# Kernel optimization log

Measured on AMD Instinct MI355X. Metric: run time of the kernel, lower is better.

## Reference

```python
import jax, jax.numpy as jnp
import numpy as np

# Model config (matches init_kwargs)
B, I, H, C = 2048, 1024, 2048, 1000   # batch, input_dim, hidden_dim, num_classes
S = 8                                  # num_wavefunctions
TOPK = 256
PARTIAL_NORM = 1.0
SM_STEPS = 2                           # self_modulation_steps
EPS = 1e-8


def setup_inputs() -> dict:
    key = jax.random.key(0)
    ks = jax.random.split(key, 9)
    x      = jax.random.normal(ks[0], (B, I), jnp.float32)
    # stacked per-wavefunction Linear(input_dim, 2*hidden_dim)
    W      = jax.random.normal(ks[1], (S, 2 * H, I), jnp.float32) * (1.0 / np.sqrt(I))
    b      = jax.random.normal(ks[2], (S, 2 * H), jnp.float32) * 0.01
    phases = jax.random.normal(ks[3], (S, H), jnp.float32) * 0.1   # phase_per_dim=True
    gate_W = jax.random.normal(ks[4], (H, H), jnp.float32) * (1.0 / np.sqrt(H))
    gate_b = jax.random.normal(ks[5], (H,), jnp.float32) * 0.01
    clf_W  = jax.random.normal(ks[6], (C, H), jnp.float32) * (1.0 / np.sqrt(H))
    clf_b  = jax.random.normal(ks[7], (C,), jnp.float32) * 0.01
    return {"x": x, "W": W, "b": b, "phases": phases,
            "gate_W": gate_W, "gate_b": gate_b, "clf_W": clf_W, "clf_b": clf_b}


def reference(x, W, b, phases, gate_W, gate_b, clf_W, clf_b):
    # All wavefunction branches batched into one GEMM: [B,S,2H]
    out = jnp.einsum('bi,shi->bsh', x, W) + b[None]
    out = jnp.exp(-(out * out))                      # ArcBell activation
    alpha, beta = out[..., :H], out[..., H:]         # [B,S,H] each
    norm_sq = jnp.sum(alpha * alpha + beta * beta, axis=-1, keepdims=True) + EPS
    factor = jnp.sqrt((PARTIAL_NORM * PARTIAL_NORM) / norm_sq)  # [B,S,1]
    alpha = alpha * factor
    beta = beta * factor
    cphi = jnp.cos(phases)[None]                     # [1,S,H]
    sphi = jnp.sin(phases)[None]
    # phase rotation + complex accumulate over wavefunctions
    sup_real = jnp.sum(alpha * cphi - beta * sphi, axis=1)   # [B,H]
    sup_imag = jnp.sum(alpha * sphi + beta * cphi, axis=1)
    # self-modulation (fixed small step count -> Python loop is fine)
    for _ in range(SM_STEPS):
        mag = jnp.sqrt(sup_real * sup_real + sup_imag * sup_imag)
        gate = jax.nn.sigmoid(mag @ gate_W.T + gate_b)
        sup_real = sup_real * gate
        sup_imag = sup_imag * gate
    mag_sq = sup_real * sup_real + sup_imag * sup_imag       # [B,H]
    # top-k masked probability aggregation
    _, idx = jax.lax.top_k(mag_sq, TOPK)                     # idx: [B,TOPK]
    mask = jnp.zeros_like(mag_sq).at[jnp.arange(B)[:, None], idx].set(1.0)
    masked = mag_sq * mask
    probs = masked / (jnp.sum(masked, axis=-1, keepdims=True) + EPS)
    logits = probs @ clf_W.T + clf_b                         # [B,C]
    return logits
```

## Files before the change

### kernel.cpp

```cpp
#include <hip/hip_runtime.h>

typedef _Float16 f16;
typedef _Float16 f16x8 __attribute__((ext_vector_type(8)));
typedef _Float16 f16x4 __attribute__((ext_vector_type(4)));
typedef float f32x4 __attribute__((ext_vector_type(4)));

#define B_    2048
#define I_    1024
#define H_    2048
#define C_    1000
#define S_    8
#define N1    32768
#define TOPK_ 256

__device__ __forceinline__ void gload16(const void* g, void* l) {
  __builtin_amdgcn_global_load_lds((const __attribute__((address_space(1))) void*)g,
                                   (__attribute__((address_space(3))) void*)l,
                                   16, 0, 0);
}

__global__ void cvt8_kernel(const float* __restrict__ src, f16* __restrict__ dst, int n8) {
  int i = blockIdx.x * blockDim.x + threadIdx.x;
  if (i >= n8) return;
  const float4 a = reinterpret_cast<const float4*>(src)[2 * i];
  const float4 b = reinterpret_cast<const float4*>(src)[2 * i + 1];
  f16x8 o = { (f16)a.x, (f16)a.y, (f16)a.z, (f16)a.w,
              (f16)b.x, (f16)b.y, (f16)b.z, (f16)b.w };
  reinterpret_cast<f16x8*>(dst)[i] = o;
}

__global__ void cvt_clf_kernel(const float* __restrict__ src, f16* __restrict__ dst) {
  int i = blockIdx.x * blockDim.x + threadIdx.x;
  if (i >= (1024 * H_ / 8)) return;
  f16x8 o;
  if (i < (C_ * H_ / 8)) {
    const float4 a = reinterpret_cast<const float4*>(src)[2 * i];
    const float4 b = reinterpret_cast<const float4*>(src)[2 * i + 1];
    o = (f16x8){ (f16)a.x, (f16)a.y, (f16)a.z, (f16)a.w,
                 (f16)b.x, (f16)b.y, (f16)b.z, (f16)b.w };
  } else {
    o = (f16x8){ (f16)0.f, (f16)0.f, (f16)0.f, (f16)0.f,
                 (f16)0.f, (f16)0.f, (f16)0.f, (f16)0.f };
  }
  reinterpret_cast<f16x8*>(dst)[i] = o;
}

__global__ void phase_kernel(const float* __restrict__ ph, float* __restrict__ c,
                             float* __restrict__ s) {
  int i = blockIdx.x * blockDim.x + threadIdx.x;
  if (i >= S_ * H_) return;
  float p = ph[i];
  c[i] = cosf(p);
  s[i] = sinf(p);
}

template<int BM, int BN, int WM, int WN, int THREADS, int EPI>
__global__ __launch_bounds__(THREADS, (THREADS == 512) ? 2 : 3)
void gemm_ring(const f16* __restrict__ A, const f16* __restrict__ Bmat,
               const int K, const int MT, const int ldc, const int nreal,
               const float* __restrict__ bias,
               f16* __restrict__ act_out,
               const float* __restrict__ magin,
               float* __restrict__ mago32, f16* __restrict__ mago16,
               float* __restrict__ msqout, float* __restrict__ logits)
{
  constexpr int MREP  = BM / (WM * 16);
  constexpr int NREP  = BN / (WN * 16);
  constexpr int CA    = (BM * 64) / (THREADS * 16);
  constexpr int CB    = (BN * 64) / (THREADS * 16);
  constexpr int CALLS = CA + CB;
  constexpr int SLOT  = (BM + BN) * 32;
  __shared__ f16 SL[4 * SLOT];

  const int tid  = threadIdx.x;
  const int lane = tid & 63, wid = tid >> 6;
  const int wr = wid / WN, wc = wid % WN;
  const int fr = lane & 15, fq = lane >> 4;

  const int nwg = gridDim.x;
  const int chunk = nwg >> 3;
  const int swz = (blockIdx.x & 7) * chunk + (blockIdx.x >> 3);
  const int mt = swz % MT, nt = swz / MT;
  const long brow = (long)mt * BM, bcol = (long)nt * BN;

  const f16* srcA[CA];
  const f16* srcB[CB];
#pragma unroll
  for (int a = 0; a < CA; ++a) {
    const int r = (a * THREADS + tid) >> 2;
    const int cs = (tid & 3) ^ ((r ^ (r >> 2)) & 3);
    srcA[a] = A + (size_t)(brow + r) * K + cs * 8;
  }
#pragma unroll
  for (int a = 0; a < CB; ++a) {
    const int r = (a * THREADS + tid) >> 2;
    const int cs = (tid & 3) ^ ((r ^ (r >> 2)) & 3);
    srcB[a] = Bmat + (size_t)(bcol + r) * K + cs * 8;
  }

  int ard[MREP], brd[NREP];
#pragma unroll
  for (int m = 0; m < MREP; ++m) {
    const int r = wr * MREP * 16 + m * 16 + fr;
    ard[m] = r * 32 + ((fq ^ ((r ^ (r >> 2)) & 3)) * 8);
  }
#pragma unroll
  for (int n = 0; n < NREP; ++n) {
    const int r = wc * NREP * 16 + n * 16 + fr;
    brd[n] = r * 32 + ((fq ^ ((r ^ (r >> 2)) & 3)) * 8);
  }

  f32x4 acc[MREP][NREP] = {};
  const int ntile = K >> 5;

#define STAGE_TILE(tt)                                                         \
  do {                                                                         \
    f16* D = &SL[((tt) & 3) * SLOT];                                           \
    const long kt = (long)(tt) * 32;                                           \
    _Pragma("unroll")                                                          \
    for (int a = 0; a < CA; ++a)                                               \
      gload16(srcA[a] + kt, D + a * THREADS * 8 + wid * 512);                  \
    _Pragma("unroll")                                                          \
    for (int a = 0; a < CB; ++a)                                               \
      gload16(srcB[a] + kt, D + BM * 32 + a * THREADS * 8 + wid * 512);        \
  } while (0)

  STAGE_TILE(0); STAGE_TILE(1); STAGE_TILE(2);

  for (int t = 0; t < ntile; ++t) {
    if (t + 3 < ntile) STAGE_TILE(t + 3);
    if (t < ntile - 3)       asm volatile("s_waitcnt vmcnt(%0)" :: "i"(3 * CALLS) : "memory");
    else if (t == ntile - 3) asm volatile("s_waitcnt vmcnt(%0)" :: "i"(2 * CALLS) : "memory");
    else if (t == ntile - 2) asm volatile("s_waitcnt vmcnt(%0)" :: "i"(1 * CALLS) : "memory");
    else                     asm volatile("s_waitcnt vmcnt(0)" ::: "memory");
    __builtin_amdgcn_s_barrier();
    asm volatile("" ::: "memory");

    const f16* SA = &SL[(t & 3) * SLOT];
    const f16* SB = SA + BM * 32;
    f16x8 af[MREP], bf[NREP];
#pragma unroll
    for (int m = 0; m < MREP; ++m) af[m] = *(const f16x8*)(SA + ard[m]);
#pragma unroll
    for (int n = 0; n < NREP; ++n) bf[n] = *(const f16x8*)(SB + brd[n]);

    __builtin_amdgcn_s_setprio(1);
#pragma unroll
    for (int m = 0; m < MREP; ++m)
#pragma unroll
      for (int n = 0; n < NREP; ++n)
        acc[m][n] = __builtin_amdgcn_mfma_f32_16x16x32_f16(af[m], bf[n], acc[m][n], 0, 0, 0);
    __builtin_amdgcn_s_setprio(0);
    asm volatile("" ::: "memory");
    __builtin_amdgcn_s_barrier();
  }
#undef STAGE_TILE

#pragma unroll
  for (int m = 0; m < MREP; ++m) {
    const long r0 = brow + wr * MREP * 16 + m * 16 + fq * 4;
#pragma unroll
    for (int n = 0; n < NREP; ++n) {
      const long c = bcol + wc * NREP * 16 + n * 16 + fr;
      float bv;
      if (EPI == 2) bv = (c < nreal) ? bias[c] : 0.f;
      else          bv = bias[c];
#pragma unroll
      for (int j = 0; j < 4; ++j) {
        const long r = r0 + j;
        const float t = acc[m][n][j] + bv;
        if (EPI == 0) {
          act_out[r * (long)ldc + c] = (f16)__expf(-t * t);
        } else if (EPI == 1) {
          const float g = 1.f / (1.f + __expf(-t));
          const long idx = r * (long)ldc + c;
          const float v = magin[idx] * g;
          if (msqout) msqout[idx] = v * v;
          else { mago32[idx] = v; mago16[idx] = (f16)v; }
        } else {
          if (c < nreal) logits[r * (long)nreal + c] = t;
        }
      }
    }
  }
}

__global__ __launch_bounds__(512)
void normsup_kernel(const f16* __restrict__ act,
                    const float* __restrict__ cphi, const float* __restrict__ sphi,
                    float* __restrict__ mag32, f16* __restrict__ mag16)
{
  __shared__ float buf[4096];
  __shared__ float red[8];
  const int b = blockIdx.x, tid = threadIdx.x;
  const int lane = tid & 63, wv = tid >> 6;
  float sr[4] = {0, 0, 0, 0}, si[4] = {0, 0, 0, 0};
  const f16* base = act + (size_t)b * N1;

  for (int s = 0; s < S_; ++s) {
    f16x8 v = *(const f16x8*)(base + s * 4096 + tid * 8);
    float ls = 0.f;
#pragma unroll
    for (int e = 0; e < 8; ++e) {
      float f = (float)v[e];
      buf[tid * 8 + e] = f;
      ls += f * f;
    }
#pragma unroll
    for (int o = 32; o > 0; o >>= 1) ls += __shfl_down(ls, o);
    if (lane == 0) red[wv] = ls;
    __syncthreads();
    const float tot = red[0] + red[1] + red[2] + red[3] + red[4] + red[5] + red[6] + red[7];
    const float factor = 1.f / sqrtf(tot + 1e-8f);

    const float4 c4 = *(const float4*)(cphi + s * H_ + tid * 4);
    const float4 s4 = *(const float4*)(sphi + s * H_ + tid * 4);
    const float4 a4 = *(const float4*)(&buf[tid * 4]);
    const float4 b4 = *(const float4*)(&buf[2048 + tid * 4]);
    sr[0] += factor * (a4.x * c4.x - b4.x * s4.x); si[0] += factor * (a4.x * s4.x + b4.x * c4.x);
    sr[1] += factor * (a4.y * c4.y - b4.y * s4.y); si[1] += factor * (a4.y * s4.y + b4.y * c4.y);
    sr[2] += factor * (a4.z * c4.z - b4.z * s4.z); si[2] += factor * (a4.z * s4.z + b4.z * c4.z);
    sr[3] += factor * (a4.w * c4.w - b4.w * s4.w); si[3] += factor * (a4.w * s4.w + b4.w * c4.w);
    __syncthreads();
  }

  const size_t o = (size_t)b * H_ + tid * 4;
  const float m0 = sqrtf(sr[0] * sr[0] + si[0] * si[0]);
  const float m1 = sqrtf(sr[1] * sr[1] + si[1] * si[1]);
  const float m2 = sqrtf(sr[2] * sr[2] + si[2] * si[2]);
  const float m3 = sqrtf(sr[3] * sr[3] + si[3] * si[3]);
  *(float4*)(mag32 + o) = make_float4(m0, m1, m2, m3);
  f16x4 mh = { (f16)m0, (f16)m1, (f16)m2, (f16)m3 };
  *(f16x4*)(mag16 + o) = mh;
}

__global__ __launch_bounds__(256)
void topk_kernel(const float* __restrict__ msq, f16* __restrict__ probs)
{
  __shared__ unsigned vals[2048];
  __shared__ int hist[256];
  __shared__ int scn[256];
  __shared__ int sdig, sknew;
  __shared__ float wsum[4];
  const int b = blockIdx.x, tid = threadIdx.x;
  const unsigned* row = (const unsigned*)(msq + (size_t)b * H_);

  uint4 v0 = *(const uint4*)(row + tid * 8);
  uint4 v1 = *(const uint4*)(row + tid * 8 + 4);
  vals[tid * 8 + 0] = v0.x; vals[tid * 8 + 1] = v0.y;
  vals[tid * 8 + 2] = v0.z; vals[tid * 8 + 3] = v0.w;
  vals[tid * 8 + 4] = v1.x; vals[tid * 8 + 5] = v1.y;
  vals[tid * 8 + 6] = v1.z; vals[tid * 8 + 7] = v1.w;
  __syncthreads();

  int k = TOPK_;
  unsigned prefix = 0, pmask = 0;
  for (int pass = 0; pass < 4; ++pass) {
    const int sh = 24 - pass * 8;
    hist[tid] = 0;
    __syncthreads();
#pragma unroll
    for (int e = 0; e < 8; ++e) {
      unsigned v = vals[tid * 8 + e];
      if ((v & pmask) == prefix) atomicAdd(&hist[(v >> sh) & 255u], 1);
    }
    __syncthreads();
    const int own = hist[tid];
    int sc = own;
    scn[tid] = sc;
    __syncthreads();
    for (int o2 = 1; o2 < 256; o2 <<= 1) {
      int add = (tid + o2 < 256) ? scn[tid + o2] : 0;
      __syncthreads();
      sc += add; scn[tid] = sc;
      __syncthreads();
    }
    if (sc >= k && (sc - own) < k) { sdig = tid; sknew = k - (sc - own); }
    __syncthreads();
    prefix |= ((unsigned)sdig) << sh;
    pmask  |= 0xFFu << sh;
    k = sknew;
    __syncthreads();
  }

  const unsigned T = prefix;
  const int krem = k;
  unsigned vl[8];
  int eqc = 0;
#pragma unroll
  for (int e = 0; e < 8; ++e) { vl[e] = vals[tid * 8 + e]; if (vl[e] == T) eqc++; }
  int sc2 = eqc;
  scn[tid] = sc2;
  __syncthreads();
  for (int o2 = 1; o2 < 256; o2 <<= 1) {
    int add = (tid >= o2) ? scn[tid - o2] : 0;
    __syncthreads();
    sc2 += add; scn[tid] = sc2;
    __syncthreads();
  }
  int rank = sc2 - eqc;
  float ls = 0.f;
  bool sel[8];
#pragma unroll
  for (int e = 0; e < 8; ++e) {
    const unsigned v = vl[e];
    bool s_ = false;
    if (v > T) s_ = true;
    else if (v == T) { s_ = (rank < krem); ++rank; }
    sel[e] = s_;
    if (s_) ls += __uint_as_float(v);
  }
#pragma unroll
  for (int o2 = 32; o2 > 0; o2 >>= 1) ls += __shfl_down(ls, o2);
  if ((tid & 63) == 0) wsum[tid >> 6] = ls;
  __syncthreads();
  const float tot = wsum[0] + wsum[1] + wsum[2] + wsum[3];
  const float inv = 1.f / (tot + 1e-8f);
  f16x8 ov;
#pragma unroll
  for (int e = 0; e < 8; ++e)
    ov[e] = sel[e] ? (f16)(__uint_as_float(vl[e]) * inv) : (f16)0.f;
  *(f16x8*)(probs + (size_t)b * H_ + tid * 8) = ov;
}

extern "C" void kernel_launch(void* const* d_in, const int* in_sizes, int n_in,
                              void* d_out, int out_size, void* d_ws, size_t ws_size,
                              hipStream_t stream)
{
  const float* x  = (const float*)d_in[0];
  const float* W  = (const float*)d_in[1];
  const float* bb = (const float*)d_in[2];
  const float* ph = (const float*)d_in[3];
  const float* gW = (const float*)d_in[4];
  const float* gb = (const float*)d_in[5];
  const float* cW = (const float*)d_in[6];
  const float* cb = (const float*)d_in[7];
  float* out = (float*)d_out;

  char* base = (char*)d_ws;
  size_t off = 0;
  auto take = [&](size_t bytes) -> char* {
    char* r = base + off;
    off += (bytes + 255) & ~(size_t)255;
    return r;
  };
  f16*   Wf    = (f16*)  take((size_t)S_ * 2 * H_ * I_ * 2);
  f16*   xf    = (f16*)  take((size_t)B_ * I_ * 2);
  f16*   gWf   = (f16*)  take((size_t)H_ * H_ * 2);
  f16*   cWf   = (f16*)  take((size_t)1024 * H_ * 2);
  float* cphi  = (float*)take((size_t)S_ * H_ * 4);
  float* sphi  = (float*)take((size_t)S_ * H_ * 4);
  f16*   act   = (f16*)  take((size_t)B_ * N1 * 2);
  float* mag0f = (float*)take((size_t)B_ * H_ * 4);
  f16*   mag0h = (f16*)  take((size_t)B_ * H_ * 2);
  float* mag1f = (float*)take((size_t)B_ * H_ * 4);
  f16*   mag1h = (f16*)  take((size_t)B_ * H_ * 2);
  float* msq   = (float*)take((size_t)B_ * H_ * 4);
  f16*   probs = (f16*)  take((size_t)B_ * H_ * 2);
  (void)ws_size; (void)in_sizes; (void)n_in; (void)out_size;

  cvt8_kernel<<<(S_ * 2 * H_ * I_ / 8 + 255) / 256, 256, 0, stream>>>(W, Wf, S_ * 2 * H_ * I_ / 8);
  cvt8_kernel<<<(B_ * I_ / 8 + 255) / 256, 256, 0, stream>>>(x, xf, B_ * I_ / 8);
  cvt8_kernel<<<(H_ * H_ / 8 + 255) / 256, 256, 0, stream>>>(gW, gWf, H_ * H_ / 8);
  cvt_clf_kernel<<<(1024 * H_ / 8 + 255) / 256, 256, 0, stream>>>(cW, cWf);
  phase_kernel<<<(S_ * H_ + 255) / 256, 256, 0, stream>>>(ph, cphi, sphi);

  gemm_ring<256, 256, 2, 4, 512, 0><<<(B_ / 256) * (N1 / 256), 512, 0, stream>>>(
      xf, Wf, I_, B_ / 256, N1, N1, bb, act,
      nullptr, nullptr, nullptr, nullptr, nullptr);

  normsup_kernel<<<B_, 512, 0, stream>>>(act, cphi, sphi, mag0f, mag0h);

  gemm_ring<128, 64, 2, 2, 256, 1><<<(B_ / 128) * (H_ / 64), 256, 0, stream>>>(
      mag0h, gWf, H_, B_ / 128, H_, H_, gb, nullptr,
      mag0f, mag1f, mag1h, nullptr, nullptr);

  gemm_ring<128, 64, 2, 2, 256, 1><<<(B_ / 128) * (H_ / 64), 256, 0, stream>>>(
      mag1h, gWf, H_, B_ / 128, H_, H_, gb, nullptr,
      mag1f, nullptr, nullptr, msq, nullptr);

  topk_kernel<<<B_, 256, 0, stream>>>(msq, probs);

  gemm_ring<128, 64, 2, 2, 256, 2><<<(B_ / 128) * (1024 / 64), 256, 0, stream>>>(
      probs, cWf, H_, B_ / 128, 0, C_, cb, nullptr,
      nullptr, nullptr, nullptr, nullptr, out);
}
```

Before: 391.9 us.

## Replace first GEMM with dedicated 8-phase double-buffered MFMA kernel

```diff
diff --git a/kernel.cpp b/kernel.cpp
--- a/kernel.cpp
+++ b/kernel.cpp
@@ -54,12 +54,141 @@
   s[i] = sinf(p);
 }
 
+__global__ __launch_bounds__(512, 2)
+void gemm1_8p(const f16* __restrict__ A, const f16* __restrict__ Bm,
+              const float* __restrict__ bias, f16* __restrict__ act)
+{
+  __shared__ char SL[131072];
+  const int tid = threadIdx.x, lane = tid & 63, wid = tid >> 6;
+  const int wr = wid >> 2, wc = wid & 3;
+  const int fr = lane & 15, fq = lane >> 4;
+  const int bid = blockIdx.x;
+  const int swz = (bid & 7) * 128 + (bid >> 3);
+  const int mt = swz & 7, nt = swz >> 3;
+  const long brow = (long)mt * 256, bcol = (long)nt * 256;
+
+  const int schunk = ((tid & 3) ^ ((tid >> 3) & 3)) * 8;
+  const f16* sA = A  + (brow + (tid >> 2)) * (long)I_ + schunk;
+  const f16* sB = Bm + (bcol + (tid >> 2)) * (long)I_ + schunk;
+
+  const int co = (fq ^ ((fr >> 1) & 3)) * 16;
+  const int rdA0 = (wr * 128 + fr) * 64 + co;
+  const int rdB0 = 32768 + (wc * 64 + fr) * 64 + co;
+
+  f32x4 acc[8][4] = {};
+
+#define STG(mat, kh, c, tp, buf)                                                \
+  gload16(((mat) ? sB : sA) + (size_t)(c) * 128 * I_ + (size_t)(tp) * 64 + (kh) * 32, \
+          SL + (buf) * 65536 + (mat) * 32768 + (kh) * 16384 + (c) * 8192 + tid * 16)
+
+  STG(0,0,0,0,0); STG(0,0,1,0,0); STG(1,0,0,0,0); STG(1,0,1,0,0);
+  STG(0,1,0,0,0); STG(0,1,1,0,0); STG(1,1,0,0,0); STG(1,1,1,0,0);
+  asm volatile("s_waitcnt vmcnt(4)" ::: "memory");
+  __builtin_amdgcn_s_barrier();
+
+#pragma unroll 1
+  for (int t = 0; t < 16; ++t) {
+    const int buf = t & 1, nbuf = buf ^ 1;
+    const char* rb = SL + buf * 65536;
+    f16x8 af[4], bf[4];
+
+    if (t < 15) { STG(0,0,0,t+1,nbuf); STG(0,0,1,t+1,nbuf);
+                  STG(1,0,0,t+1,nbuf); STG(1,0,1,t+1,nbuf); }
+#pragma unroll
+    for (int n = 0; n < 4; ++n) bf[n] = *(const f16x8*)(rb + rdB0 + n * 1024);
+#pragma unroll
+    for (int i = 0; i < 4; ++i) af[i] = *(const f16x8*)(rb + rdA0 + i * 1024);
+    asm volatile("" ::: "memory");
+    __builtin_amdgcn_s_barrier();
+    __builtin_amdgcn_sched_barrier(0);
+    __builtin_amdgcn_s_setprio(1);
+#pragma unroll
+    for (int i = 0; i < 4; ++i)
+#pragma unroll
+      for (int n = 0; n < 4; ++n)
+        acc[i][n] = __builtin_amdgcn_mfma_f32_16x16x32_f16(af[i], bf[n], acc[i][n], 0, 0, 0);
+    __builtin_amdgcn_s_setprio(0);
+    __builtin_amdgcn_sched_barrier(0);
+    __builtin_amdgcn_s_barrier();
+
+#pragma unroll
+    for (int i = 0; i < 4; ++i) af[i] = *(const f16x8*)(rb + rdA0 + (4 + i) * 1024);
+    asm volatile("" ::: "memory");
+    __builtin_amdgcn_s_barrier();
+    __builtin_amdgcn_sched_barrier(0);
+    __builtin_amdgcn_s_setprio(1);
+#pragma unroll
+    for (int i = 0; i < 4; ++i)
+#pragma unroll
+      for (int n = 0; n < 4; ++n)
+        acc[4 + i][n] = __builtin_amdgcn_mfma_f32_16x16x32_f16(af[i], bf[n], acc[4 + i][n], 0, 0, 0);
+    __builtin_amdgcn_s_setprio(0);
+    __builtin_amdgcn_sched_barrier(0);
+    if (t < 15) asm volatile("s_waitcnt vmcnt(4)" ::: "memory");
+    else        asm volatile("s_waitcnt vmcnt(0)" ::: "memory");
+    __builtin_amdgcn_s_barrier();
+
+    if (t < 15) { STG(0,1,0,t+1,nbuf); STG(0,1,1,t+1,nbuf);
+                  STG(1,1,0,t+1,nbuf); STG(1,1,1,t+1,nbuf); }
+#pragma unroll
+    for (int n = 0; n < 4; ++n) bf[n] = *(const f16x8*)(rb + 16384 + rdB0 + n * 1024);
+#pragma unroll
+    for (int i = 0; i < 4; ++i) af[i] = *(const f16x8*)(rb + 16384 + rdA0 + i * 1024);
+    asm volatile("" ::: "memory");
+    __builtin_amdgcn_s_barrier();
+    __builtin_amdgcn_sched_barrier(0);
+    __builtin_amdgcn_s_setprio(1);
+#pragma unroll
+    for (int i = 0; i < 4; ++i)
+#pragma unroll
+      for (int n = 0; n < 4; ++n)
+        acc[i][n] = __builtin_amdgcn_mfma_f32_16x16x32_f16(af[i], bf[n], acc[i][n], 0, 0, 0);
+    __builtin_amdgcn_s_setprio(0);
+    __builtin_amdgcn_sched_barrier(0);
+    __builtin_amdgcn_s_barrier();
+
+#pragma unroll
+    for (int i = 0; i < 4; ++i) af[i] = *(const f16x8*)(rb + 16384 + rdA0 + (4 + i) * 1024);
+    asm volatile("" ::: "memory");
+    __builtin_amdgcn_s_barrier();
+    __builtin_amdgcn_sched_barrier(0);
+    __builtin_amdgcn_s_setprio(1);
+#pragma unroll
+    for (int i = 0; i < 4; ++i)
+#pragma unroll
+      for (int n = 0; n < 4; ++n)
+        acc[4 + i][n] = __builtin_amdgcn_mfma_f32_16x16x32_f16(af[i], bf[n], acc[4 + i][n], 0, 0, 0);
+    __builtin_amdgcn_s_setprio(0);
+    __builtin_amdgcn_sched_barrier(0);
+    if (t < 15) asm volatile("s_waitcnt vmcnt(4)" ::: "memory");
+    else        asm volatile("s_waitcnt vmcnt(0)" ::: "memory");
+    __builtin_amdgcn_s_barrier();
+  }
+#undef STG
+
+  float bv[4];
+#pragma unroll
+  for (int n = 0; n < 4; ++n) bv[n] = bias[bcol + wc * 64 + n * 16 + fr];
+#pragma unroll
+  for (int m = 0; m < 8; ++m) {
+    const long r0 = brow + wr * 128 + m * 16 + fq * 4;
+#pragma unroll
+    for (int n = 0; n < 4; ++n) {
+      const long c = bcol + wc * 64 + n * 16 + fr;
+#pragma unroll
+      for (int j = 0; j < 4; ++j) {
+        const float tt = acc[m][n][j] + bv[n];
+        act[(r0 + j) * (long)N1 + c] = (f16)__expf(-tt * tt);
+      }
+    }
+  }
+}
+
 template<int BM, int BN, int WM, int WN, int THREADS, int EPI>
-__global__ __launch_bounds__(THREADS, (THREADS == 512) ? 2 : 3)
+__global__ __launch_bounds__(THREADS, 3)
 void gemm_ring(const f16* __restrict__ A, const f16* __restrict__ Bmat,
                const int K, const int MT, const int ldc, const int nreal,
                const float* __restrict__ bias,
-               f16* __restrict__ act_out,
                const float* __restrict__ magin,
                float* __restrict__ mago32, f16* __restrict__ mago16,
                float* __restrict__ msqout, float* __restrict__ logits)
@@ -169,9 +298,7 @@
       for (int j = 0; j < 4; ++j) {
         const long r = r0 + j;
         const float t = acc[m][n][j] + bv;
-        if (EPI == 0) {
-          act_out[r * (long)ldc + c] = (f16)__expf(-t * t);
-        } else if (EPI == 1) {
+        if (EPI == 1) {
           const float g = 1.f / (1.f + __expf(-t));
           const long idx = r * (long)ldc + c;
           const float v = magin[idx] * g;
@@ -365,23 +492,21 @@
   cvt_clf_kernel<<<(1024 * H_ / 8 + 255) / 256, 256, 0, stream>>>(cW, cWf);
   phase_kernel<<<(S_ * H_ + 255) / 256, 256, 0, stream>>>(ph, cphi, sphi);
 
-  gemm_ring<256, 256, 2, 4, 512, 0><<<(B_ / 256) * (N1 / 256), 512, 0, stream>>>(
-      xf, Wf, I_, B_ / 256, N1, N1, bb, act,
-      nullptr, nullptr, nullptr, nullptr, nullptr);
+  gemm1_8p<<<(B_ / 256) * (N1 / 256), 512, 0, stream>>>(xf, Wf, bb, act);
 
   normsup_kernel<<<B_, 512, 0, stream>>>(act, cphi, sphi, mag0f, mag0h);
 
   gemm_ring<128, 64, 2, 2, 256, 1><<<(B_ / 128) * (H_ / 64), 256, 0, stream>>>(
-      mag0h, gWf, H_, B_ / 128, H_, H_, gb, nullptr,
+      mag0h, gWf, H_, B_ / 128, H_, H_, gb,
       mag0f, mag1f, mag1h, nullptr, nullptr);
 
   gemm_ring<128, 64, 2, 2, 256, 1><<<(B_ / 128) * (H_ / 64), 256, 0, stream>>>(
-      mag1h, gWf, H_, B_ / 128, H_, H_, gb, nullptr,
+      mag1h, gWf, H_, B_ / 128, H_, H_, gb,
       mag1f, nullptr, nullptr, msq, nullptr);
 
   topk_kernel<<<B_, 256, 0, stream>>>(msq, probs);
 
   gemm_ring<128, 64, 2, 2, 256, 2><<<(B_ / 128) * (1024 / 64), 256, 0, stream>>>(
-      probs, cWf, H_, B_ / 128, 0, C_, cb, nullptr,
+      probs, cWf, H_, B_ / 128, 0, C_, cb,
       nullptr, nullptr, nullptr, nullptr, out);
 }
```

Result: faster. 380.5 us (-2.9%).
